# Kernel optimization log

Measured on AMD Instinct MI355X. Metric: run time of the kernel, lower is better.

Reference implementation:

```python
import jax, jax.numpy as jnp
import numpy as np

BATCH = 16384
MAX_ACTIVE = 32
FEAT = 768
HIDDEN = 1024


def setup_inputs() -> dict:
    key = jax.random.key(0)
    k1, k2, k3, k4, k5, k6 = jax.random.split(key, 6)
    stm = jax.random.randint(k1, (BATCH, MAX_ACTIVE), 0, FEAT, dtype=jnp.int32)
    nstm = jax.random.randint(k2, (BATCH, MAX_ACTIVE), 0, FEAT, dtype=jnp.int32)
    # Linear params (PyTorch layout: weight is (out_features, in_features))
    ft_w = jax.random.normal(k3, (HIDDEN, FEAT), dtype=jnp.float32) * 0.05
    ft_b = jax.random.normal(k4, (HIDDEN,), dtype=jnp.float32) * 0.05
    out_w = jax.random.normal(k5, (1, 2 * HIDDEN), dtype=jnp.float32) * 0.05
    out_b = jax.random.normal(k6, (1,), dtype=jnp.float32) * 0.05
    return {"stm": stm, "nstm": nstm, "ft_w": ft_w, "ft_b": ft_b,
            "out_w": out_w, "out_b": out_b}


def sparse_to_dense(indices: jnp.ndarray, size: int = FEAT) -> jnp.ndarray:
    """(B, max_active) int indices with -1 padding -> (B, size) 0/1 float32."""
    b = indices.shape[0]
    valid = (indices >= 0).astype(jnp.float32)          # (B, A)
    cols = jnp.clip(indices, 0, size - 1)               # padded -> col 0, masked by `valid`
    rows = jnp.arange(b, dtype=jnp.int32)[:, None]      # (B, 1) broadcast
    dense = jnp.zeros((b, size), dtype=jnp.float32)
    # .max matches torch's set-to-1 semantics even if duplicate indices occur
    return dense.at[rows, cols].max(valid)


def reference(stm, nstm, ft_w, ft_b, out_w, out_b):
    stm_d = sparse_to_dense(stm)                        # (B, 768)
    nstm_d = sparse_to_dense(nstm)                      # (B, 768)
    stm_h = stm_d @ ft_w.T + ft_b                       # (B, H)
    nstm_h = nstm_d @ ft_w.T + ft_b                     # (B, H)
    hidden = jnp.concatenate([stm_h, nstm_h], axis=1)   # (B, 2H)
    hidden = jnp.clip(hidden, 0.0, 1.0)
    return jax.nn.sigmoid(hidden @ out_w.T + out_b)     # (B, 1)
```

## Files before the change

kernel.cpp:

```cpp
#include <hip/hip_runtime.h>
#include <hip/hip_bf16.h>
#include <stdint.h>

#define BATCH 16384
#define MAXA 32
#define FEAT 768
#define HIDDEN 1024

__global__ __launch_bounds__(256) void scale_k(const float* __restrict__ ftw,
                                               float* __restrict__ scale,
                                               float* __restrict__ invsc,
                                               uint8_t* __restrict__ wQ) {
  if (blockIdx.x == HIDDEN) {
    if (threadIdx.x < 64) {
      uint4 v; v.x = v.y = v.z = v.w = 0x80808080u;
      ((uint4*)(wQ + (size_t)FEAT * HIDDEN))[threadIdx.x] = v;
    }
    return;
  }
  const int h = blockIdx.x;
  float a = 0.f;
#pragma unroll
  for (int p = 0; p < 3; ++p)
    a = fmaxf(a, fabsf(ftw[h * FEAT + p * 256 + threadIdx.x]));
#pragma unroll
  for (int off = 32; off > 0; off >>= 1)
    a = fmaxf(a, __shfl_xor(a, off, 64));
  __shared__ float red[4];
  if ((threadIdx.x & 63) == 0) red[threadIdx.x >> 6] = a;
  __syncthreads();
  if (threadIdx.x == 0) {
    float m = fmaxf(fmaxf(red[0], red[1]), fmaxf(red[2], red[3]));
    m = fmaxf(m, 1e-20f);
    scale[h] = m / 127.f;
    invsc[h] = 127.f / m;
  }
}

__global__ __launch_bounds__(256) void tilequant(const float* __restrict__ ftw,
                                                 const float* __restrict__ invsc,
                                                 uint8_t* __restrict__ wQ) {
  const int f0 = (blockIdx.x % (FEAT / 64)) * 64;
  const int h0 = (blockIdx.x / (FEAT / 64)) * 64;
  __shared__ uint8_t tile[64][80];
  __shared__ float inv[64];
  if (threadIdx.x < 64) inv[threadIdx.x] = invsc[h0 + threadIdx.x];
  __syncthreads();
  const int ff = threadIdx.x & 63;
  const int hb = threadIdx.x >> 6;
#pragma unroll
  for (int p = 0; p < 16; ++p) {
    int hh = p * 4 + hb;
    float w = ftw[(size_t)(h0 + hh) * FEAT + f0 + ff];
    int q = __float2int_rn(w * inv[hh]);
    tile[ff][hh] = (uint8_t)(q + 128);
  }
  __syncthreads();
  const int fs = threadIdx.x >> 2, part = threadIdx.x & 3;
  uint4 v = *(const uint4*)&tile[fs][part * 16];
  *(uint4*)(wQ + (size_t)(f0 + fs) * HIDDEN + h0 + part * 16) = v;
}

__device__ __forceinline__ void acc16(uint32_t* acc, uint4 w) {
  acc[0] += __builtin_amdgcn_perm(0u, w.x, 0x0c010c00u);
  acc[1] += __builtin_amdgcn_perm(0u, w.x, 0x0c030c02u);
  acc[2] += __builtin_amdgcn_perm(0u, w.y, 0x0c010c00u);
  acc[3] += __builtin_amdgcn_perm(0u, w.y, 0x0c030c02u);
  acc[4] += __builtin_amdgcn_perm(0u, w.z, 0x0c010c00u);
  acc[5] += __builtin_amdgcn_perm(0u, w.z, 0x0c030c02u);
  acc[6] += __builtin_amdgcn_perm(0u, w.w, 0x0c010c00u);
  acc[7] += __builtin_amdgcn_perm(0u, w.w, 0x0c030c02u);
}

__global__ __launch_bounds__(256) void nn_fwd(
    const int* __restrict__ stm, const int* __restrict__ nstm,
    const uint8_t* __restrict__ wQ, const float* __restrict__ scale,
    const float* __restrict__ bias, const float* __restrict__ outw,
    const float* __restrict__ outb, float* __restrict__ out)
{
  const int lane = threadIdx.x & 63;
  const int row  = blockIdx.x * 4 + (threadIdx.x >> 6);
  const int half = lane >> 5;
  const int pos  = lane & 31;

  const int* __restrict__ src = half ? nstm : stm;
  int idx = src[row * MAXA + pos];
  bool valid = idx >= 0;
#pragma unroll
  for (int j = 0; j < 31; ++j) {
    int other = __shfl(idx, (half << 5) | j, 64);
    if (j < pos && other == idx) valid = false;
  }
  const int fmap = valid ? idx : FEAT;

  uint32_t accs[8], accn[8];
#pragma unroll
  for (int k = 0; k < 8; ++k) { accs[k] = 0u; accn[k] = 0u; }

#pragma unroll
  for (int j = 0; j < 32; ++j) {
    int fs_ = __builtin_amdgcn_readlane(fmap, j);
    int fn_ = __builtin_amdgcn_readlane(fmap, 32 + j);
    const uint4* ps = (const uint4*)(wQ + (size_t)fs_ * HIDDEN);
    const uint4* pn = (const uint4*)(wQ + (size_t)fn_ * HIDDEN);
    uint4 ws_ = ps[lane];
    uint4 wn_ = pn[lane];
    acc16(accs, ws_);
    acc16(accn, wn_);
  }

  const int DB = 32 * 128;

  const int hbase = lane * 16;
  float sc[16], bb[16], ows[16], own[16];
  {
    const float4* s4 = (const float4*)(scale + hbase);
    const float4* b4 = (const float4*)(bias + hbase);
    const float4* oS = (const float4*)(outw + hbase);
    const float4* oN = (const float4*)(outw + HIDDEN + hbase);
#pragma unroll
    for (int q = 0; q < 4; ++q) {
      float4 v;
      v = s4[q]; sc[4*q]=v.x; sc[4*q+1]=v.y; sc[4*q+2]=v.z; sc[4*q+3]=v.w;
      v = b4[q]; bb[4*q]=v.x; bb[4*q+1]=v.y; bb[4*q+2]=v.z; bb[4*q+3]=v.w;
      v = oS[q]; ows[4*q]=v.x; ows[4*q+1]=v.y; ows[4*q+2]=v.z; ows[4*q+3]=v.w;
      v = oN[q]; own[4*q]=v.x; own[4*q+1]=v.y; own[4*q+2]=v.z; own[4*q+3]=v.w;
    }
  }
  float partial = 0.f;
#pragma unroll
  for (int k = 0; k < 16; ++k) {
    uint32_t as = accs[k >> 1], an = accn[k >> 1];
    int qs = (int)((k & 1) ? (as >> 16) : (as & 0xffffu)) - DB;
    int qn = (int)((k & 1) ? (an >> 16) : (an & 0xffffu)) - DB;
    float hs = fminf(fmaxf(fmaf((float)qs, sc[k], bb[k]), 0.f), 1.f);
    float hn = fminf(fmaxf(fmaf((float)qn, sc[k], bb[k]), 0.f), 1.f);
    partial += hs * ows[k] + hn * own[k];
  }
#pragma unroll
  for (int off = 32; off > 0; off >>= 1)
    partial += __shfl_down(partial, off, 64);
  if (lane == 0) {
    float y = partial + outb[0];
    out[row] = 1.f / (1.f + __expf(-y));
  }
}

extern "C" void kernel_launch(void* const* d_in, const int* in_sizes, int n_in,
                              void* d_out, int out_size, void* d_ws, size_t ws_size,
                              hipStream_t stream) {
  const int*   stm  = (const int*)d_in[0];
  const int*   nstm = (const int*)d_in[1];
  const float* ftw  = (const float*)d_in[2];
  const float* ftb  = (const float*)d_in[3];
  const float* outw = (const float*)d_in[4];
  const float* outb = (const float*)d_in[5];

  uint8_t* wQ    = (uint8_t*)d_ws;
  float*   scale = (float*)(wQ + (size_t)(FEAT + 1) * HIDDEN);
  float*   invsc = scale + HIDDEN;

  scale_k<<<HIDDEN + 1, 256, 0, stream>>>(ftw, scale, invsc, wQ);
  tilequant<<<(FEAT / 64) * (HIDDEN / 64), 256, 0, stream>>>(ftw, invsc, wQ);
  nn_fwd<<<BATCH / 4, 256, 0, stream>>>(stm, nstm, wQ, scale, ftb, outw, outb,
                                        (float*)d_out);
}
```

Before: 120.5 us.

## Fuse weight quantization into one kernel and software-pipeline gather loads

Merges the scale computation and transposed int8 quantization into a single kernel that handles 8 hidden rows per block and keeps each row's weights in registers, which drops one launch and a pass over global memory. In the main forward kernel, weight-row gathers are prefetched 8 deep in a rotating register buffer so load latency overlaps the byte accumulation. The kernel also gets an occupancy hint of 3 blocks per CU. The extra buffered registers could reduce occupancy or cause spills, and the quant kernel now writes 8-byte chunks per feature row instead of 16-byte chunks.

```diff
diff --git a/kernel.cpp b/kernel.cpp
--- a/kernel.cpp
+++ b/kernel.cpp
@@ -1,5 +1,4 @@
 #include <hip/hip_runtime.h>
-#include <hip/hip_bf16.h>
 #include <stdint.h>
 
 #define BATCH 16384
@@ -7,58 +6,46 @@
 #define FEAT 768
 #define HIDDEN 1024
 
-__global__ __launch_bounds__(256) void scale_k(const float* __restrict__ ftw,
-                                               float* __restrict__ scale,
-                                               float* __restrict__ invsc,
-                                               uint8_t* __restrict__ wQ) {
-  if (blockIdx.x == HIDDEN) {
-    if (threadIdx.x < 64) {
-      uint4 v; v.x = v.y = v.z = v.w = 0x80808080u;
-      ((uint4*)(wQ + (size_t)FEAT * HIDDEN))[threadIdx.x] = v;
-    }
-    return;
+__global__ __launch_bounds__(256) void prep_quant(const float* __restrict__ ftw,
+                                                  uint8_t* __restrict__ wQ,
+                                                  float* __restrict__ scale) {
+  const int h0 = blockIdx.x * 8;
+  const int hloc = threadIdx.x >> 5;
+  const int l32 = threadIdx.x & 31;
+  const int h = h0 + hloc;
+
+  float w[24];
+  float amax = 0.f;
+  const float* __restrict__ src = ftw + (size_t)h * FEAT;
+#pragma unroll
+  for (int k = 0; k < 24; ++k) {
+    w[k] = src[l32 + 32 * k];
+    amax = fmaxf(amax, fabsf(w[k]));
   }
-  const int h = blockIdx.x;
-  float a = 0.f;
 #pragma unroll
-  for (int p = 0; p < 3; ++p)
-    a = fmaxf(a, fabsf(ftw[h * FEAT + p * 256 + threadIdx.x]));
+  for (int m = 1; m <= 16; m <<= 1)
+    amax = fmaxf(amax, __shfl_xor(amax, m, 64));
+  amax = fmaxf(amax, 1e-20f);
+  if (l32 == 0) scale[h] = amax / 127.f;
+  const float inv = 127.f / amax;
+
+  __shared__ __align__(16) uint8_t tile[FEAT * 8];
 #pragma unroll
-  for (int off = 32; off > 0; off >>= 1)
-    a = fmaxf(a, __shfl_xor(a, off, 64));
-  __shared__ float red[4];
-  if ((threadIdx.x & 63) == 0) red[threadIdx.x >> 6] = a;
-  __syncthreads();
-  if (threadIdx.x == 0) {
-    float m = fmaxf(fmaxf(red[0], red[1]), fmaxf(red[2], red[3]));
-    m = fmaxf(m, 1e-20f);
-    scale[h] = m / 127.f;
-    invsc[h] = 127.f / m;
-  }
-}
-
-__global__ __launch_bounds__(256) void tilequant(const float* __restrict__ ftw,
-                                                 const float* __restrict__ invsc,
-                                                 uint8_t* __restrict__ wQ) {
-  const int f0 = (blockIdx.x % (FEAT / 64)) * 64;
-  const int h0 = (blockIdx.x / (FEAT / 64)) * 64;
-  __shared__ uint8_t tile[64][80];
-  __shared__ float inv[64];
-  if (threadIdx.x < 64) inv[threadIdx.x] = invsc[h0 + threadIdx.x];
-  __syncthreads();
-  const int ff = threadIdx.x & 63;
-  const int hb = threadIdx.x >> 6;
-#pragma unroll
-  for (int p = 0; p < 16; ++p) {
-    int hh = p * 4 + hb;
-    float w = ftw[(size_t)(h0 + hh) * FEAT + f0 + ff];
-    int q = __float2int_rn(w * inv[hh]);
-    tile[ff][hh] = (uint8_t)(q + 128);
+  for (int k = 0; k < 24; ++k) {
+    int q = __float2int_rn(w[k] * inv);
+    tile[(l32 + 32 * k) * 8 + hloc] = (uint8_t)(q + 128);
   }
   __syncthreads();
-  const int fs = threadIdx.x >> 2, part = threadIdx.x & 3;
-  uint4 v = *(const uint4*)&tile[fs][part * 16];
-  *(uint4*)(wQ + (size_t)(f0 + fs) * HIDDEN + h0 + part * 16) = v;
+
+#pragma unroll
+  for (int p = 0; p < 3; ++p) {
+    int f = threadIdx.x + 256 * p;
+    unsigned long long v = *(const unsigned long long*)&tile[f * 8];
+    *(unsigned long long*)(wQ + (size_t)f * HIDDEN + h0) = v;
+  }
+
+  if (blockIdx.x == 0)
+    ((uint32_t*)(wQ + (size_t)FEAT * HIDDEN))[threadIdx.x] = 0x80808080u;
 }
 
 __device__ __forceinline__ void acc16(uint32_t* acc, uint4 w) {
@@ -72,7 +59,7 @@
   acc[7] += __builtin_amdgcn_perm(0u, w.w, 0x0c030c02u);
 }
 
-__global__ __launch_bounds__(256) void nn_fwd(
+__global__ __launch_bounds__(256, 3) void nn_fwd(
     const int* __restrict__ stm, const int* __restrict__ nstm,
     const uint8_t* __restrict__ wQ, const float* __restrict__ scale,
     const float* __restrict__ bias, const float* __restrict__ outw,
@@ -97,14 +84,24 @@
 #pragma unroll
   for (int k = 0; k < 8; ++k) { accs[k] = 0u; accn[k] = 0u; }
 
+  uint4 bs[8], bn[8];
+#pragma unroll
+  for (int j = 0; j < 8; ++j) {
+    int fs_ = __builtin_amdgcn_readlane(fmap, j);
+    int fn_ = __builtin_amdgcn_readlane(fmap, 32 + j);
+    bs[j] = ((const uint4*)(wQ + (size_t)fs_ * HIDDEN))[lane];
+    bn[j] = ((const uint4*)(wQ + (size_t)fn_ * HIDDEN))[lane];
+  }
 #pragma unroll
   for (int j = 0; j < 32; ++j) {
-    int fs_ = __builtin_amdgcn_readlane(fmap, j);
-    int fn_ = __builtin_amdgcn_readlane(fmap, 32 + j);
-    const uint4* ps = (const uint4*)(wQ + (size_t)fs_ * HIDDEN);
-    const uint4* pn = (const uint4*)(wQ + (size_t)fn_ * HIDDEN);
-    uint4 ws_ = ps[lane];
-    uint4 wn_ = pn[lane];
+    uint4 ws_ = bs[j & 7];
+    uint4 wn_ = bn[j & 7];
+    if (j < 24) {
+      int fs_ = __builtin_amdgcn_readlane(fmap, j + 8);
+      int fn_ = __builtin_amdgcn_readlane(fmap, 32 + j + 8);
+      bs[j & 7] = ((const uint4*)(wQ + (size_t)fs_ * HIDDEN))[lane];
+      bn[j & 7] = ((const uint4*)(wQ + (size_t)fn_ * HIDDEN))[lane];
+    }
     acc16(accs, ws_);
     acc16(accn, wn_);
   }
@@ -158,10 +155,8 @@
 
   uint8_t* wQ    = (uint8_t*)d_ws;
   float*   scale = (float*)(wQ + (size_t)(FEAT + 1) * HIDDEN);
-  float*   invsc = scale + HIDDEN;
 
-  scale_k<<<HIDDEN + 1, 256, 0, stream>>>(ftw, scale, invsc, wQ);
-  tilequant<<<(FEAT / 64) * (HIDDEN / 64), 256, 0, stream>>>(ftw, invsc, wQ);
+  prep_quant<<<HIDDEN / 8, 256, 0, stream>>>(ftw, wQ, scale);
   nn_fwd<<<BATCH / 4, 256, 0, stream>>>(stm, nstm, wQ, scale, ftb, outw, outb,
                                         (float*)d_out);
 }
```

After: 117.2 us. 2.7% less time.
